# Kernel tuning notes

Hardware: AMD Instinct MI355X
Metric: run time of the kernel (lower is better)

The kernel has to match this reference:

```python
import jax, jax.numpy as jnp
import numpy as np

N_NODES = 50000
SEQ_LEN = 20
INPUT_DIM = 16
HIDDEN = 128
LATENT = 64
N_EDGES = 800000


def setup_inputs() -> dict:
    key = jax.random.key(0)
    ks = iter(jax.random.split(key, 64))
    def p(shape, scale=0.05):
        return jax.random.normal(next(ks), shape, dtype=jnp.float32) * scale
    inp = {}
    inp['track_sequences'] = jax.random.normal(next(ks), (N_NODES, SEQ_LEN, INPUT_DIM), dtype=jnp.float32)
    inp['edge_index'] = jax.random.randint(next(ks), (2, N_EDGES), 0, N_NODES, dtype=jnp.int64)
    # LSTM (2 layers, torch gate order i,f,g,o)
    inp['lstm_Wih0'] = p((4 * HIDDEN, INPUT_DIM)); inp['lstm_Whh0'] = p((4 * HIDDEN, HIDDEN))
    inp['lstm_bih0'] = p((4 * HIDDEN,));            inp['lstm_bhh0'] = p((4 * HIDDEN,))
    inp['lstm_Wih1'] = p((4 * HIDDEN, HIDDEN));     inp['lstm_Whh1'] = p((4 * HIDDEN, HIDDEN))
    inp['lstm_bih1'] = p((4 * HIDDEN,));            inp['lstm_bhh1'] = p((4 * HIDDEN,))
    # encoder MLP: hidden->hidden->latent
    inp['enc_W1'] = p((HIDDEN, HIDDEN)); inp['enc_b1'] = p((HIDDEN,))
    inp['enc_W2'] = p((HIDDEN, LATENT)); inp['enc_b2'] = p((LATENT,))
    # 3 GCN layers
    inp['gcn_W0'] = p((LATENT, HIDDEN)); inp['gcn_b0'] = p((HIDDEN,))
    inp['gcn_W1'] = p((HIDDEN, HIDDEN)); inp['gcn_b1'] = p((HIDDEN,))
    inp['gcn_W2'] = p((HIDDEN, HIDDEN)); inp['gcn_b2'] = p((HIDDEN,))
    # edge predictor MLP: 2H -> H -> H/2 -> 1 (sigmoid)
    inp['e_W1'] = p((2 * HIDDEN, HIDDEN)); inp['e_b1'] = p((HIDDEN,))
    inp['e_W2'] = p((HIDDEN, HIDDEN // 2)); inp['e_b2'] = p((HIDDEN // 2,))
    inp['e_W3'] = p((HIDDEN // 2, 1)); inp['e_b3'] = p((1,))
    # classifier: H -> H/2 -> 4
    inp['c_W1'] = p((HIDDEN, HIDDEN // 2)); inp['c_b1'] = p((HIDDEN // 2,))
    inp['c_W2'] = p((HIDDEN // 2, 4)); inp['c_b2'] = p((4,))
    # uncertainty: H -> H/2 -> 1 (softplus)
    inp['u_W1'] = p((HIDDEN, HIDDEN // 2)); inp['u_b1'] = p((HIDDEN // 2,))
    inp['u_W2'] = p((HIDDEN // 2, 1)); inp['u_b2'] = p((1,))
    return inp


def _lstm_layer(x, Wih, Whh, bih, bhh):
    # x: [N, T, Din]; torch gate order i, f, g, o
    n, t, _ = x.shape
    h_dim = Whh.shape[1]
    xg = jnp.einsum('ntd,gd->ntg', x, Wih) + bih  # [N, T, 4H] precomputed input part
    def step(carry, xt):
        h, c = carry
        g = xt + h @ Whh.T + bhh
        i, f, gg, o = jnp.split(g, 4, axis=-1)
        c = jax.nn.sigmoid(f) * c + jax.nn.sigmoid(i) * jnp.tanh(gg)
        h = jax.nn.sigmoid(o) * jnp.tanh(c)
        return (h, c), h
    h0 = jnp.zeros((n, h_dim), x.dtype)
    (_, _), hs = jax.lax.scan(step, (h0, h0), jnp.swapaxes(xg, 0, 1))
    return jnp.swapaxes(hs, 0, 1)  # [N, T, H]


def _gcn(x, W, b, src, dst, num_nodes):
    # PyG GCNConv: self-loops, symmetric deg^-1/2 normalization
    x = x @ W  # [N, out]
    loop = jnp.arange(num_nodes, dtype=src.dtype)
    s = jnp.concatenate([src, loop])
    d = jnp.concatenate([dst, loop])
    deg = jax.ops.segment_sum(jnp.ones_like(d, x.dtype), d, num_segments=num_nodes)
    dinv = jax.lax.rsqrt(jnp.maximum(deg, 1.0))  # deg >= 1 due to self-loops
    norm = dinv[s] * dinv[d]  # [E+N]
    out = jax.ops.segment_sum(x[s] * norm[:, None], d, num_segments=num_nodes)
    return out + b


def reference(track_sequences, edge_index,
              lstm_Wih0, lstm_Whh0, lstm_bih0, lstm_bhh0,
              lstm_Wih1, lstm_Whh1, lstm_bih1, lstm_bhh1,
              enc_W1, enc_b1, enc_W2, enc_b2,
              gcn_W0, gcn_b0, gcn_W1, gcn_b1, gcn_W2, gcn_b2,
              e_W1, e_b1, e_W2, e_b2, e_W3, e_b3,
              c_W1, c_b1, c_W2, c_b2,
              u_W1, u_b1, u_W2, u_b2):
    n = track_sequences.shape[0]
    # --- TrackEncoder (eval mode: LSTM inter-layer dropout inactive) ---
    h = _lstm_layer(track_sequences, lstm_Wih0, lstm_Whh0, lstm_bih0, lstm_bhh0)
    h = _lstm_layer(h, lstm_Wih1, lstm_Whh1, lstm_bih1, lstm_bhh1)
    final_hidden = h[:, -1]  # [N, H]
    latent = jax.nn.relu(final_hidden @ enc_W1 + enc_b1) @ enc_W2 + enc_b2  # [N, L]
    # --- GCN stack (eval mode: dropout inactive) ---
    src, dst = edge_index[0], edge_index[1]
    x = latent
    for W, b in ((gcn_W0, gcn_b0), (gcn_W1, gcn_b1), (gcn_W2, gcn_b2)):
        x = jax.nn.relu(_gcn(x, W, b, src, dst, n))
    # --- edge predictor ---
    ef = jnp.concatenate([x[src], x[dst]], axis=1)  # [E, 2H]
    ef = jax.nn.relu(ef @ e_W1 + e_b1)
    ef = jax.nn.relu(ef @ e_W2 + e_b2)
    edge_pred = jax.nn.sigmoid(ef @ e_W3 + e_b3)  # [E, 1]
    # --- classifier & uncertainty heads ---
    track_classes = jax.nn.relu(x @ c_W1 + c_b1) @ c_W2 + c_b2  # [N, 4]
    uncertainties = jax.nn.softplus(jax.nn.relu(x @ u_W1 + u_b1) @ u_W2 + u_b2)  # [N, 1]
    return (x, edge_pred, track_classes, uncertainties)
```

## Files before the change

### kernel.cpp

```cpp
#include <hip/hip_runtime.h>
#include <math.h>

typedef float f32x4 __attribute__((ext_vector_type(4)));
typedef short s16x8 __attribute__((ext_vector_type(8)));
typedef unsigned short u16;

__device__ __forceinline__ float sigmoid_(float x) { return 1.f / (1.f + __expf(-x)); }
__device__ __forceinline__ float tanh_(float x) {
  float e = __expf(-2.f * x);
  return fmaf(2.f, 1.f / (1.f + e), -1.f);
}
__device__ __forceinline__ float softplus_(float x) {
  return (x > 15.f) ? x : log1pf(__expf(x));
}
__device__ __forceinline__ u16 f2bf(float f) {
  unsigned u = __float_as_uint(f);
  u += 0x7fffu + ((u >> 16) & 1u);
  return (u16)(u >> 16);
}
__device__ __forceinline__ float bf2f(u16 u) {
  return __uint_as_float((unsigned)u << 16);
}
#define PIN4(x) asm volatile("" : "+v"(x))

__global__ void prep_lstm_w(const float* __restrict__ Wih0, const float* __restrict__ Whh0,
                            const float* __restrict__ Wih1, const float* __restrict__ Whh1,
                            const float* __restrict__ bih0, const float* __restrict__ bhh0,
                            const float* __restrict__ bih1, const float* __restrict__ bhh1,
                            u16* __restrict__ Wp0, u16* __restrict__ Wp1,
                            float* __restrict__ bs0, float* __restrict__ bs1)
{
  int idx = blockIdx.x * 256 + threadIdx.x;
  if (idx < 20 * 512 * 8) {
    int c = idx >> 12, rem = idx & 4095;
    int col = rem >> 3, e = rem & 7;
    int k = c * 8 + e;
    float v = 0.f;
    if (k < 16) v = Wih0[col * 16 + k];
    else if (k >= 32) v = Whh0[col * 128 + (k - 32)];
    Wp0[idx] = f2bf(v);
  }
  int i1 = idx - 20 * 512 * 8;
  if (i1 >= 0 && i1 < 32 * 512 * 8) {
    int c = i1 >> 12, rem = i1 & 4095;
    int col = rem >> 3, e = rem & 7;
    int k = c * 8 + e;
    float v = (k < 128) ? Wih1[col * 128 + k] : Whh1[col * 128 + (k - 128)];
    Wp1[i1] = f2bf(v);
  }
  int i2 = idx - 52 * 512 * 8;
  if (i2 >= 0 && i2 < 512) bs0[i2] = bih0[i2] + bhh0[i2];
  int i3 = i2 - 512;
  if (i3 >= 0 && i3 < 512) bs1[i3] = bih1[i3] + bhh1[i3];
}

__global__ void pack_w(const float* __restrict__ W, u16* __restrict__ Wp, int K, int C) {
  int idx = blockIdx.x * 256 + threadIdx.x;
  if (idx < K * C) {
    int k = idx / C, col = idx % C;
    Wp[((size_t)(k >> 3) * C + col) * 8 + (k & 7)] = f2bf(W[idx]);
  }
}

__global__ void pack_headw(const float* __restrict__ cW1, const float* __restrict__ cb1,
                           const float* __restrict__ cW2, const float* __restrict__ cb2,
                           const float* __restrict__ uW1, const float* __restrict__ ub1,
                           const float* __restrict__ uW2, const float* __restrict__ ub2,
                           u16* __restrict__ cuW1p, float* __restrict__ cub1,
                           u16* __restrict__ cuW2p, float* __restrict__ cub2)
{
  int idx = blockIdx.x * 256 + threadIdx.x;
  if (idx < 128 * 128) {
    int k = idx >> 7, col = idx & 127;
    float v = (col < 64) ? cW1[k * 64 + col] : uW1[k * 64 + (col - 64)];
    cuW1p[((size_t)(k >> 3) * 128 + col) * 8 + (k & 7)] = f2bf(v);
  }
  int j = idx - 128 * 128;
  if (j >= 0 && j < 2048) {
    int ch = j >> 7, rem = j & 127, col = rem >> 3, e = rem & 7;
    int k = ch * 8 + e;
    float v = 0.f;
    if (col < 4 && k < 64) v = cW2[k * 4 + col];
    else if (col == 4 && k >= 64) v = uW2[k - 64];
    cuW2p[j] = f2bf(v);
  }
  int j2 = idx - (128 * 128 + 2048);
  if (j2 >= 0 && j2 < 128) cub1[j2] = (j2 < 64) ? cb1[j2] : ub1[j2 - 64];
  int j3 = j2 - 128;
  if (j3 >= 0 && j3 < 16) cub2[j3] = (j3 < 4) ? cb2[j3] : (j3 == 4 ? ub2[0] : 0.f);
}

__device__ __forceinline__ void epi2(const f32x4 (&acc)[2][4], f32x4* cs,
    const float (&bs)[4], u16* ldsw, int uoff, int kq, int mh,
    int nodebase, float* hf, int u, int n, bool last)
{
#pragma unroll
  for (int mm = 0; mm < 2; ++mm) {
#pragma unroll
    for (int r = 0; r < 4; ++r) {
      float gi = acc[mm][0][r] + bs[0];
      float gf = acc[mm][1][r] + bs[1];
      float gg = acc[mm][2][r] + bs[2];
      float go = acc[mm][3][r] + bs[3];
      float c = sigmoid_(gf) * cs[mm][r] + sigmoid_(gi) * tanh_(gg);
      cs[mm][r] = c;
      float h = sigmoid_(go) * tanh_(c);
      int node = (mh * 2 + mm) * 16 + kq * 4 + r;
      ldsw[uoff + node * 8] = f2bf(h);
      if (last) {
        int gn = nodebase + node;
        if (gn < n) hf[(size_t)gn * 128 + u] = h;
      }
    }
  }
}

__global__ __launch_bounds__(512, 2) void lstm_l0(
    const float* __restrict__ seq, const u16* __restrict__ Wp0,
    const float* __restrict__ bs0, u16* __restrict__ h0seq,
    int n, int tile0, int ntiles)
{
  __shared__ __align__(16) u16 A0[2 * 20 * 512];
  const int RSZ = 20 * 512;
  const int tid = threadIdx.x;
  const int l = tid & 63;
  const int wq = __builtin_amdgcn_readfirstlane(tid >> 6);
  const int kq = l >> 4;
  const int la = (l & 15) * 8;
  const int colu = wq * 16 + (l & 15);
  const int uoff = (4 + (colu >> 3)) * 512 + (colu & 7);

  s16x8 b0[5][4];
#pragma unroll
  for (int kc = 0; kc < 5; ++kc)
#pragma unroll
    for (int g = 0; g < 4; ++g) {
      b0[kc][g] = *(const s16x8*)&Wp0[(size_t)(kc * 4 + kq) * 4096 + (g * 128 + colu) * 8];
      PIN4(b0[kc][g]);
    }
  float bsr[4];
#pragma unroll
  for (int g = 0; g < 4; ++g) bsr[g] = bs0[g * 128 + colu];
  const f32x4 zero4 = {0.f, 0.f, 0.f, 0.f};

  for (int tt = blockIdx.x; tt < ntiles; tt += gridDim.x) {
    const int nodebase = (tile0 + tt) * 64;
    const int nld = min(nodebase + (tid >> 2), n - 1);
    u16* __restrict__ hdst = h0seq + (size_t)tt * 20 * 8192;
    for (int i = tid; i < 18 * 512; i += 512) A0[2 * 512 + i] = 0;
    for (int i = tid; i < 2 * 512; i += 512) A0[RSZ + 2 * 512 + i] = 0;
    if (tid < 256) {
      int nd = tid >> 2, q = tid & 3;
      f32x4 v = __builtin_nontemporal_load((const f32x4*)(seq + (size_t)nld * 320 + q * 4));
      unsigned d0 = (unsigned)f2bf(v[0]) | ((unsigned)f2bf(v[1]) << 16);
      unsigned d1 = (unsigned)f2bf(v[2]) | ((unsigned)f2bf(v[3]) << 16);
      unsigned* dstp = (unsigned*)&A0[(q >> 1) * 512 + nd * 8 + (q & 1) * 4];
      dstp[0] = d0; dstp[1] = d1;
    }
    f32x4 c0[4];
#pragma unroll
    for (int m = 0; m < 4; ++m) c0[m] = zero4;
    __syncthreads();

    for (int t = 0; t < 20; ++t) {
      const int base_r = (t & 1) * RSZ;
      const int base_w = ((t + 1) & 1) * RSZ;
      f32x4 xnext;
      const bool ldx = (t < 19) && (tid < 256);
      if (ldx) xnext = __builtin_nontemporal_load(
          (const f32x4*)(seq + (size_t)nld * 320 + (t + 1) * 16 + (tid & 3) * 4));
      if (t >= 1) {
        s16x8 u0 = *(const s16x8*)&A0[base_r + 2048 + tid * 8];
        s16x8 u1 = *(const s16x8*)&A0[base_r + 2048 + 4096 + tid * 8];
        __builtin_nontemporal_store(u0, (s16x8*)&hdst[(size_t)(t - 1) * 8192 + tid * 8]);
        __builtin_nontemporal_store(u1, (s16x8*)&hdst[(size_t)(t - 1) * 8192 + 4096 + tid * 8]);
      }
#pragma unroll
      for (int mh = 0; mh < 2; ++mh) {
        f32x4 acc[2][4];
#pragma unroll
        for (int mm = 0; mm < 2; ++mm)
#pragma unroll
          for (int g = 0; g < 4; ++g) acc[mm][g] = zero4;
#pragma unroll
        for (int kc = 0; kc < 5; ++kc) {
          const int ch = kc * 4 + kq;
          s16x8 av[2];
#pragma unroll
          for (int mm = 0; mm < 2; ++mm)
            av[mm] = *(const s16x8*)&A0[base_r + ch * 512 + (mh * 2 + mm) * 128 + la];
#pragma unroll
          for (int g = 0; g < 4; ++g)
#pragma unroll
            for (int mm = 0; mm < 2; ++mm)
              acc[mm][g] = __builtin_amdgcn_mfma_f32_16x16x32_bf16(av[mm], b0[kc][g], acc[mm][g], 0, 0, 0);
        }
        epi2(acc, &c0[mh * 2], bsr, &A0[base_w], uoff, kq, mh, 0, nullptr, colu, 0, false);
      }
      if (ldx) {
        int nd = tid >> 2, q = tid & 3;
        unsigned d0 = (unsigned)f2bf(xnext[0]) | ((unsigned)f2bf(xnext[1]) << 16);
        unsigned d1 = (unsigned)f2bf(xnext[2]) | ((unsigned)f2bf(xnext[3]) << 16);
        unsigned* dstp = (unsigned*)&A0[base_w + (q >> 1) * 512 + nd * 8 + (q & 1) * 4];
        dstp[0] = d0; dstp[1] = d1;
      }
      __syncthreads();
    }
    {
      s16x8 u0 = *(const s16x8*)&A0[2048 + tid * 8];
      s16x8 u1 = *(const s16x8*)&A0[2048 + 4096 + tid * 8];
      __builtin_nontemporal_store(u0, (s16x8*)&hdst[(size_t)19 * 8192 + tid * 8]);
      __builtin_nontemporal_store(u1, (s16x8*)&hdst[(size_t)19 * 8192 + 4096 + tid * 8]);
    }
    __syncthreads();
  }
}

__global__ __launch_bounds__(512, 2) void lstm_l1(
    const u16* __restrict__ h0seq, const u16* __restrict__ Wp1,
    const float* __restrict__ bs1, float* __restrict__ hfinal,
    int n, int tile0, int ntiles)
{
  __shared__ __align__(16) u16 A1[2 * 32 * 512];
  const int RSZ = 32 * 512;
  const int tid = threadIdx.x;
  const int l = tid & 63;
  const int wq = __builtin_amdgcn_readfirstlane(tid >> 6);
  const int kq = l >> 4;
  const int la = (l & 15) * 8;
  const int colu = wq * 16 + (l & 15);
  const int uoff = (16 + (colu >> 3)) * 512 + (colu & 7);

  s16x8 b1[8][4];
#pragma unroll
  for (int kc = 0; kc < 8; ++kc)
#pragma unroll
    for (int g = 0; g < 4; ++g) {
      b1[kc][g] = *(const s16x8*)&Wp1[(size_t)(kc * 4 + kq) * 4096 + (g * 128 + colu) * 8];
      PIN4(b1[kc][g]);
    }
  float bsr[4];
#pragma unroll
  for (int g = 0; g < 4; ++g) bsr[g] = bs1[g * 128 + colu];
  const f32x4 zero4 = {0.f, 0.f, 0.f, 0.f};

  for (int tt = blockIdx.x; tt < ntiles; tt += gridDim.x) {
    const int nodebase = (tile0 + tt) * 64;
    const u16* __restrict__ hsrc = h0seq + (size_t)tt * 20 * 8192;
    for (int i = tid; i < 16 * 512; i += 512) A1[16 * 512 + i] = 0;
    {
      s16x8 s0 = __builtin_nontemporal_load((const s16x8*)&hsrc[tid * 8]);
      s16x8 s1 = __builtin_nontemporal_load((const s16x8*)&hsrc[4096 + tid * 8]);
      *(s16x8*)&A1[tid * 8] = s0;
      *(s16x8*)&A1[4096 + tid * 8] = s1;
    }
    f32x4 c1[4];
#pragma unroll
    for (int m = 0; m < 4; ++m) c1[m] = zero4;
    __syncthreads();

    for (int t = 0; t < 20; ++t) {
      const int base_r = (t & 1) * RSZ;
      const int base_w = ((t + 1) & 1) * RSZ;
      s16x8 p0, p1;
      const bool ld = (t < 19);
      if (ld) {
        p0 = __builtin_nontemporal_load((const s16x8*)&hsrc[(size_t)(t + 1) * 8192 + tid * 8]);
        p1 = __builtin_nontemporal_load((const s16x8*)&hsrc[(size_t)(t + 1) * 8192 + 4096 + tid * 8]);
      }
#pragma unroll
      for (int mh = 0; mh < 2; ++mh) {
        f32x4 acc[2][4];
#pragma unroll
        for (int mm = 0; mm < 2; ++mm)
#pragma unroll
          for (int g = 0; g < 4; ++g) acc[mm][g] = zero4;
#pragma unroll
        for (int kc = 0; kc < 8; ++kc) {
          const int ch = kc * 4 + kq;
          s16x8 av[2];
#pragma unroll
          for (int mm = 0; mm < 2; ++mm)
            av[mm] = *(const s16x8*)&A1[base_r + ch * 512 + (mh * 2 + mm) * 128 + la];
#pragma unroll
          for (int g = 0; g < 4; ++g)
#pragma unroll
            for (int mm = 0; mm < 2; ++mm)
              acc[mm][g] = __builtin_amdgcn_mfma_f32_16x16x32_bf16(av[mm], b1[kc][g], acc[mm][g], 0, 0, 0);
        }
        epi2(acc, &c1[mh * 2], bsr, &A1[base_w], uoff, kq, mh, nodebase, hfinal, colu, n, t == 19);
      }
      if (ld) {
        *(s16x8*)&A1[base_w + tid * 8] = p0;
        *(s16x8*)&A1[base_w + 4096 + tid * 8] = p1;
      }
      __syncthreads();
    }
  }
}

template<int KD, int COLS, bool INBF, bool OUTBF, bool RELU, bool BIAS>
__global__ __launch_bounds__(COLS * 4, 4) void ngemm_m(
    const void* __restrict__ xin_, const u16* __restrict__ Wp,
    const float* __restrict__ b, void* __restrict__ out_, int n)
{
  constexpr int NT = COLS * 4;
  __shared__ __align__(16) u16 A[(KD / 8) * 512];
  const int tid = threadIdx.x;
  const int l = tid & 63;
  const int wq = __builtin_amdgcn_readfirstlane(tid >> 6);
  const int kq = l >> 4;
  const int la = (l & 15) * 8;
  const int colu = wq * 16 + (l & 15);
  const int nodebase = blockIdx.x * 64;

  for (int s = tid; s < 64 * KD / 8; s += NT) {
    int nd = s / (KD / 8), q = s % (KD / 8);
    int gn = min(nodebase + nd, n - 1);
    if (INBF) {
      const u16* xp = (const u16*)xin_ + (size_t)gn * KD + q * 8;
      *(s16x8*)&A[q * 512 + nd * 8] = *(const s16x8*)xp;
    } else {
      const float* xp = (const float*)xin_ + (size_t)gn * KD + q * 8;
      float4 v0 = *(const float4*)xp;
      float4 v1 = *(const float4*)(xp + 4);
      s16x8 pk;
      pk[0] = (short)f2bf(v0.x); pk[1] = (short)f2bf(v0.y);
      pk[2] = (short)f2bf(v0.z); pk[3] = (short)f2bf(v0.w);
      pk[4] = (short)f2bf(v1.x); pk[5] = (short)f2bf(v1.y);
      pk[6] = (short)f2bf(v1.z); pk[7] = (short)f2bf(v1.w);
      *(s16x8*)&A[q * 512 + nd * 8] = pk;
    }
  }
  __syncthreads();

  const f32x4 zero4 = {0.f, 0.f, 0.f, 0.f};
  f32x4 acc[4];
#pragma unroll
  for (int m = 0; m < 4; ++m) acc[m] = zero4;
#pragma unroll
  for (int kc = 0; kc < KD / 32; ++kc) {
    const int ch = kc * 4 + kq;
    s16x8 bv = *(const s16x8*)&Wp[((size_t)ch * COLS + colu) * 8];
#pragma unroll
    for (int m = 0; m < 4; ++m) {
      s16x8 av = *(const s16x8*)&A[ch * 512 + m * 128 + la];
      acc[m] = __builtin_amdgcn_mfma_f32_16x16x32_bf16(av, bv, acc[m], 0, 0, 0);
    }
  }
  float bb = BIAS ? b[colu] : 0.f;
#pragma unroll
  for (int m = 0; m < 4; ++m)
#pragma unroll
    for (int r = 0; r < 4; ++r) {
      int gn = nodebase + m * 16 + kq * 4 + r;
      if (gn < n) {
        float v = acc[m][r] + bb;
        if (RELU) v = fmaxf(v, 0.f);
        if (OUTBF) ((u16*)out_)[(size_t)gn * COLS + colu] = f2bf(v);
        else       ((float*)out_)[(size_t)gn * COLS + colu] = v;
      }
    }
}

__global__ void deg_count(const int* __restrict__ dst, float* __restrict__ deg, int ne, int n) {
  int i = blockIdx.x * 256 + threadIdx.x;
  if (i < ne) {
    int d = dst[i]; d = min(max(d, 0), n - 1);
    atomicAdd(deg + d, 1.f);
  }
}

__global__ void dinv_k(const float* __restrict__ deg, float* __restrict__ dinv, int n) {
  int i = blockIdx.x * 256 + threadIdx.x;
  if (i < n) dinv[i] = rsqrtf(deg[i] + 1.f);
}

__global__ void scan_part(const float* __restrict__ deg, int* __restrict__ part, int n) {
  __shared__ int sh[256];
  const int tid = threadIdx.x;
  const int base = blockIdx.x * 1024;
  int s = 0;
  for (int j = tid; j < 1024; j += 256) {
    int i = base + j;
    s += (i < n) ? (int)deg[i] : 0;
  }
  sh[tid] = s;
  __syncthreads();
  for (int off = 128; off > 0; off >>= 1) {
    if (tid < off) sh[tid] += sh[tid + off];
    __syncthreads();
  }
  if (tid == 0) part[blockIdx.x] = sh[0];
}

__global__ void scan_exc(int* __restrict__ part, int nb, int* __restrict__ rowptr, int n) {
  __shared__ int sh[256];
  const int tid = threadIdx.x;
  int v = (tid < nb) ? part[tid] : 0;
  sh[tid] = v;
  __syncthreads();
  for (int off = 1; off < 256; off <<= 1) {
    int t = (tid >= off) ? sh[tid - off] : 0;
    __syncthreads();
    sh[tid] += t;
    __syncthreads();
  }
  if (tid < nb) part[tid] = sh[tid] - v;
  if (tid == 255) rowptr[n] = sh[255];
}

__global__ void scan_final(const float* __restrict__ deg, const int* __restrict__ part,
                           int* __restrict__ rowptr, int n) {
  __shared__ int sh[1024];
  const int tid = threadIdx.x;
  const int i = blockIdx.x * 1024 + tid;
  int v = (i < n) ? (int)deg[i] : 0;
  sh[tid] = v;
  __syncthreads();
  for (int off = 1; off < 1024; off <<= 1) {
    int t = (tid >= off) ? sh[tid - off] : 0;
    __syncthreads();
    sh[tid] += t;
    __syncthreads();
  }
  if (i < n) rowptr[i] = part[blockIdx.x] + sh[tid] - v;
}

__global__ void fill_k(const int* __restrict__ src, const int* __restrict__ dst,
                       const int* __restrict__ rowptr, int* __restrict__ cursor,
                       const float* __restrict__ dinv,
                       int* __restrict__ cidx, float* __restrict__ enrm, int ne, int n) {
  int i = blockIdx.x * 256 + threadIdx.x;
  if (i < ne) {
    int s = min(max(src[i], 0), n - 1);
    int d = min(max(dst[i], 0), n - 1);
    int p = atomicAdd(cursor + d, 1);
    int o = rowptr[d] + p;
    cidx[o] = s;
    enrm[o] = dinv[s] * dinv[d];
  }
}

template<bool OUT32>
__global__ __launch_bounds__(256, 4) void gcn_gather_bf(
    const u16* __restrict__ y, const int* __restrict__ rowptr,
    const int* __restrict__ cidx, const float* __restrict__ enrm,
    const float* __restrict__ dinv, const float* __restrict__ b,
    void* __restrict__ out, int n)
{
  const int l = threadIdx.x & 63;
  const int wq = threadIdx.x >> 6;
  const int node = blockIdx.x * 4 + wq;
  if (node >= n) return;
  float dv = dinv[node];
  unsigned su = ((const unsigned*)(y + (size_t)node * 128))[l];
  float ax = bf2f((u16)(su & 0xffff)) * dv * dv;
  float ay = bf2f((u16)(su >> 16)) * dv * dv;
  int r0 = rowptr[node], r1 = rowptr[node + 1];
  int e = r0;
  for (; e + 1 < r1; e += 2) {
    int s0 = cidx[e], s1 = cidx[e + 1];
    float n0 = enrm[e], n1 = enrm[e + 1];
    unsigned u0 = ((const unsigned*)(y + (size_t)s0 * 128))[l];
    unsigned u1 = ((const unsigned*)(y + (size_t)s1 * 128))[l];
    ax = fmaf(n0, bf2f((u16)(u0 & 0xffff)), ax);
    ay = fmaf(n0, bf2f((u16)(u0 >> 16)), ay);
    ax = fmaf(n1, bf2f((u16)(u1 & 0xffff)), ax);
    ay = fmaf(n1, bf2f((u16)(u1 >> 16)), ay);
  }
  if (e < r1) {
    int s0 = cidx[e];
    float n0 = enrm[e];
    unsigned u0 = ((const unsigned*)(y + (size_t)s0 * 128))[l];
    ax = fmaf(n0, bf2f((u16)(u0 & 0xffff)), ax);
    ay = fmaf(n0, bf2f((u16)(u0 >> 16)), ay);
  }
  float2 bb = *(const float2*)(b + l * 2);
  float ox = fmaxf(ax + bb.x, 0.f);
  float oy = fmaxf(ay + bb.y, 0.f);
  if (OUT32) {
    float2 o; o.x = ox; o.y = oy;
    *(float2*)((float*)out + (size_t)node * 128 + l * 2) = o;
  } else {
    unsigned pk = (unsigned)f2bf(ox) | ((unsigned)f2bf(oy) << 16);
    ((unsigned*)((u16*)out + (size_t)node * 128))[l] = pk;
  }
}

__global__ __launch_bounds__(256, 4) void gather64_k(
    const float* __restrict__ y, const int* __restrict__ rowptr,
    const int* __restrict__ cidx, const float* __restrict__ enrm,
    const float* __restrict__ dinv, float* __restrict__ out, int n)
{
  const int l = threadIdx.x & 63;
  const int wq = threadIdx.x >> 6;
  const int node = blockIdx.x * 4 + wq;
  if (node >= n) return;
  float dv = dinv[node];
  float acc = y[(size_t)node * 64 + l] * dv * dv;
  int r0 = rowptr[node], r1 = rowptr[node + 1];
  int e = r0;
  for (; e + 1 < r1; e += 2) {
    int s0 = cidx[e], s1 = cidx[e + 1];
    float n0 = enrm[e], n1 = enrm[e + 1];
    acc = fmaf(n0, y[(size_t)s0 * 64 + l], acc);
    acc = fmaf(n1, y[(size_t)s1 * 64 + l], acc);
  }
  if (e < r1) acc = fmaf(enrm[e], y[(size_t)cidx[e] * 64 + l], acc);
  out[(size_t)node * 64 + l] = acc;
}

__global__ __launch_bounds__(256, 4) void edge_head_m(
    const u16* __restrict__ P, const u16* __restrict__ Q,
    const int* __restrict__ src, const int* __restrict__ dst,
    const float* __restrict__ b1, const u16* __restrict__ eW2p,
    const float* __restrict__ b2, const float* __restrict__ eW3,
    const float* __restrict__ b3, float* __restrict__ ep, int ne, int n)
{
  __shared__ __align__(16) u16 H1f[16 * 512];
  __shared__ float Hpart[64][4];
  const int tid = threadIdx.x;
  const int l = tid & 63;
  const int w = __builtin_amdgcn_readfirstlane(tid >> 6);
  const int kq = l >> 4;
  const int la = (l & 15) * 8;
  const int col = w * 16 + (l & 15);
  const int e0 = blockIdx.x * 64;
  {
    int el = tid >> 2, q = tid & 3;
    int e = min(e0 + el, ne - 1);
    int s = min(max(src[e], 0), n - 1);
    int d = min(max(dst[e], 0), n - 1);
    const u16* pr = P + (size_t)s * 128 + q * 32;
    const u16* qr = Q + (size_t)d * 128 + q * 32;
#pragma unroll
    for (int c = 0; c < 4; ++c) {
      s16x8 pv = *(const s16x8*)(pr + c * 8);
      s16x8 qv = *(const s16x8*)(qr + c * 8);
      s16x8 hv;
#pragma unroll
      for (int i = 0; i < 8; ++i) {
        float h = bf2f((u16)pv[i]) + bf2f((u16)qv[i]) + b1[q * 32 + c * 8 + i];
        hv[i] = (short)f2bf(fmaxf(h, 0.f));
      }
      *(s16x8*)&H1f[(q * 4 + c) * 512 + el * 8] = hv;
    }
  }
  __syncthreads();
  const f32x4 zero4 = {0.f, 0.f, 0.f, 0.f};
  f32x4 acc[4];
#pragma unroll
  for (int m = 0; m < 4; ++m) acc[m] = zero4;
#pragma unroll
  for (int kc = 0; kc < 4; ++kc) {
    int ch = kc * 4 + kq;
    s16x8 bv = *(const s16x8*)&eW2p[((size_t)ch * 64 + col) * 8];
#pragma unroll
    for (int m = 0; m < 4; ++m) {
      s16x8 av = *(const s16x8*)&H1f[ch * 512 + m * 128 + la];
      acc[m] = __builtin_amdgcn_mfma_f32_16x16x32_bf16(av, bv, acc[m], 0, 0, 0);
    }
  }
  const float w3 = eW3[col];
  const float b2c = b2[col];
#pragma unroll
  for (int m = 0; m < 4; ++m)
#pragma unroll
    for (int r = 0; r < 4; ++r) {
      float v = fmaxf(acc[m][r] + b2c, 0.f) * w3;
      v += __shfl_xor(v, 1);
      v += __shfl_xor(v, 2);
      v += __shfl_xor(v, 4);
      v += __shfl_xor(v, 8);
      if ((l & 15) == 0) Hpart[m * 16 + kq * 4 + r][w] = v;
    }
  __syncthreads();
  if (tid < 64) {
    float s = Hpart[tid][0] + Hpart[tid][1] + Hpart[tid][2] + Hpart[tid][3] + b3[0];
    int e = e0 + tid;
    if (e < ne) ep[e] = 1.f / (1.f + __expf(-s));
  }
}

__global__ __launch_bounds__(512, 2) void node_heads_m(
    const float* __restrict__ x, const u16* __restrict__ cuW1p,
    const float* __restrict__ cub1, const u16* __restrict__ cuW2p,
    const float* __restrict__ cub2, float* __restrict__ cls,
    float* __restrict__ unc, int n)
{
  __shared__ __align__(16) u16 A[16 * 512];
  __shared__ __align__(16) u16 Hf[16 * 512];
  const int tid = threadIdx.x;
  const int l = tid & 63;
  const int wq = __builtin_amdgcn_readfirstlane(tid >> 6);
  const int kq = l >> 4;
  const int la = (l & 15) * 8;
  const int col = wq * 16 + (l & 15);
  const int nodebase = blockIdx.x * 64;

  for (int s = tid; s < 1024; s += 512) {
    int nd = s >> 4, q = s & 15;
    int gn = min(nodebase + nd, n - 1);
    const float* xp = x + (size_t)gn * 128 + q * 8;
    float4 v0 = *(const float4*)xp;
    float4 v1 = *(const float4*)(xp + 4);
    s16x8 pk;
    pk[0] = (short)f2bf(v0.x); pk[1] = (short)f2bf(v0.y);
    pk[2] = (short)f2bf(v0.z); pk[3] = (short)f2bf(v0.w);
    pk[4] = (short)f2bf(v1.x); pk[5] = (short)f2bf(v1.y);
    pk[6] = (short)f2bf(v1.z); pk[7] = (short)f2bf(v1.w);
    *(s16x8*)&A[q * 512 + nd * 8] = pk;
  }
  __syncthreads();

  const f32x4 zero4 = {0.f, 0.f, 0.f, 0.f};
  f32x4 acc[4];
#pragma unroll
  for (int m = 0; m < 4; ++m) acc[m] = zero4;
#pragma unroll
  for (int kc = 0; kc < 4; ++kc) {
    int ch = kc * 4 + kq;
    s16x8 bv = *(const s16x8*)&cuW1p[((size_t)ch * 128 + col) * 8];
#pragma unroll
    for (int m = 0; m < 4; ++m) {
      s16x8 av = *(const s16x8*)&A[ch * 512 + m * 128 + la];
      acc[m] = __builtin_amdgcn_mfma_f32_16x16x32_bf16(av, bv, acc[m], 0, 0, 0);
    }
  }
  const float bb = cub1[col];
#pragma unroll
  for (int m = 0; m < 4; ++m)
#pragma unroll
    for (int r = 0; r < 4; ++r) {
      float h = fmaxf(acc[m][r] + bb, 0.f);
      int node_r = m * 16 + kq * 4 + r;
      Hf[(col >> 3) * 512 + node_r * 8 + (col & 7)] = f2bf(h);
    }
  __syncthreads();
  if (wq == 0) {
    f32x4 a2[4];
#pragma unroll
    for (int m = 0; m < 4; ++m) a2[m] = zero4;
    const int col2 = l & 15;
#pragma unroll
    for (int kc = 0; kc < 4; ++kc) {
      int ch = kc * 4 + kq;
      s16x8 bv = *(const s16x8*)&cuW2p[((size_t)ch * 16 + col2) * 8];
#pragma unroll
      for (int m = 0; m < 4; ++m) {
        s16x8 av = *(const s16x8*)&Hf[ch * 512 + m * 128 + la];
        a2[m] = __builtin_amdgcn_mfma_f32_16x16x32_bf16(av, bv, a2[m], 0, 0, 0);
      }
    }
    const float b2v = cub2[col2];
#pragma unroll
    for (int m = 0; m < 4; ++m)
#pragma unroll
      for (int r = 0; r < 4; ++r) {
        int node = nodebase + m * 16 + kq * 4 + r;
        if (node < n) {
          float v = a2[m][r] + b2v;
          if (col2 < 4) cls[(size_t)node * 4 + col2] = v;
          else if (col2 == 4) unc[node] = softplus_(v);
        }
      }
  }
}

extern "C" void kernel_launch(void* const* d_in, const int* in_sizes, int n_in,
                              void* d_out, int out_size, void* d_ws, size_t ws_size,
                              hipStream_t stream)
{
  const float* seq   = (const float*)d_in[0];
  const int*   eidx  = (const int*)d_in[1];
  const float* Wih0  = (const float*)d_in[2];
  const float* Whh0  = (const float*)d_in[3];
  const float* bih0  = (const float*)d_in[4];
  const float* bhh0  = (const float*)d_in[5];
  const float* Wih1  = (const float*)d_in[6];
  const float* Whh1  = (const float*)d_in[7];
  const float* bih1  = (const float*)d_in[8];
  const float* bhh1  = (const float*)d_in[9];
  const float* encW1 = (const float*)d_in[10];
  const float* encb1 = (const float*)d_in[11];
  const float* encW2 = (const float*)d_in[12];
  const float* encb2 = (const float*)d_in[13];
  const float* gW0   = (const float*)d_in[14];
  const float* gb0   = (const float*)d_in[15];
  const float* gW1   = (const float*)d_in[16];
  const float* gb1   = (const float*)d_in[17];
  const float* gW2   = (const float*)d_in[18];
  const float* gb2   = (const float*)d_in[19];
  const float* eW1   = (const float*)d_in[20];
  const float* eb1   = (const float*)d_in[21];
  const float* eW2   = (const float*)d_in[22];
  const float* eb2   = (const float*)d_in[23];
  const float* eW3   = (const float*)d_in[24];
  const float* eb3   = (const float*)d_in[25];
  const float* cW1   = (const float*)d_in[26];
  const float* cb1   = (const float*)d_in[27];
  const float* cW2   = (const float*)d_in[28];
  const float* cb2   = (const float*)d_in[29];
  const float* uW1   = (const float*)d_in[30];
  const float* ub1   = (const float*)d_in[31];
  const float* uW2   = (const float*)d_in[32];
  const float* ub2   = (const float*)d_in[33];

  const int n  = in_sizes[0] / 320;
  const int ne = in_sizes[1] / 2;
  const int* src = eidx;
  const int* dst = eidx + ne;

  char* ws = (char*)d_ws;
  size_t off = 0;
  auto alloc = [&](size_t elems) -> float* {
    float* p = (float*)(ws + off);
    off += ((elems * 4 + 255) & ~(size_t)255);
    return p;
  };
  const size_t nb = (size_t)n * 128;
  float* B1     = alloc(nb);
  float* B2     = alloc(nb);
  float* B4     = alloc(nb);
  float* latent = alloc((size_t)n * 64);
  float* deg    = alloc(n);
  float* dinv   = alloc(n);
  int*   rowptr = (int*)alloc(n + 1);
  int*   cursor = (int*)alloc(n);
  int*   part   = (int*)alloc(256);
  int*   cidx   = (int*)alloc(ne);
  float* enrm   = alloc(ne);
  u16* Wp0    = (u16*)alloc(20 * 512 * 8 / 2);
  u16* Wp1    = (u16*)alloc(32 * 512 * 8 / 2);
  u16* encW1p = (u16*)alloc(128 * 128 / 2);
  u16* encW2p = (u16*)alloc(128 * 64 / 2);
  u16* gW0p   = (u16*)alloc(64 * 128 / 2);
  u16* gW1p   = (u16*)alloc(128 * 128 / 2);
  u16* gW2p   = (u16*)alloc(128 * 128 / 2);
  u16* eW1tp  = (u16*)alloc(128 * 128 / 2);
  u16* eW1bp  = (u16*)alloc(128 * 128 / 2);
  u16* eW2p   = (u16*)alloc(128 * 64 / 2);
  u16* cuW1p  = (u16*)alloc(128 * 128 / 2);
  u16* cuW2p  = (u16*)alloc(1024);
  float* cub1  = alloc(128);
  float* cub2  = alloc(16);
  float* bsum0 = alloc(512);
  float* bsum1 = alloc(512);
  (void)n_in; (void)out_size;

  float* xout = (float*)d_out;
  float* ep   = xout + nb;
  float* cls  = ep + ne;
  float* unc  = cls + (size_t)n * 4;

  auto PK = [&](const float* s, u16* d, int K, int C) {
    pack_w<<<dim3((K * C + 255) / 256), dim3(256), 0, stream>>>(s, d, K, C);
  };
  PK(encW1, encW1p, 128, 128);
  PK(encW2, encW2p, 128, 64);
  PK(gW0,   gW0p,   64, 128);
  PK(gW1,   gW1p,   128, 128);
  PK(gW2,   gW2p,   128, 128);
  PK(eW1,             eW1tp, 128, 128);
  PK(eW1 + 128 * 128, eW1bp, 128, 128);
  PK(eW2,   eW2p,   128, 64);
  pack_headw<<<dim3((128 * 128 + 2048 + 128 + 16 + 255) / 256), dim3(256), 0, stream>>>(
      cW1, cb1, cW2, cb2, uW1, ub1, uW2, ub2, cuW1p, cub1, cuW2p, cub2);

  prep_lstm_w<<<dim3((52 * 512 * 8 + 1024 + 255) / 256), dim3(256), 0, stream>>>(
      Wih0, Whh0, Wih1, Whh1, bih0, bhh0, bih1, bhh1, Wp0, Wp1, bsum0, bsum1);

  hipMemsetAsync(deg, 0, (size_t)n * 4, stream);
  deg_count<<<dim3((ne + 255) / 256), dim3(256), 0, stream>>>(dst, deg, ne, n);
  dinv_k<<<dim3((n + 255) / 256), dim3(256), 0, stream>>>(deg, dinv, n);
  const int nsb = (n + 1023) / 1024;
  scan_part<<<dim3(nsb), dim3(256), 0, stream>>>(deg, part, n);
  scan_exc<<<dim3(1), dim3(256), 0, stream>>>(part, nsb, rowptr, n);
  scan_final<<<dim3(nsb), dim3(1024), 0, stream>>>(deg, part, rowptr, n);
  hipMemsetAsync(cursor, 0, (size_t)n * 4, stream);
  fill_k<<<dim3((ne + 255) / 256), dim3(256), 0, stream>>>(
      src, dst, rowptr, cursor, dinv, cidx, enrm, ne, n);

  const int nblk = (n + 63) / 64;
  const int ntiles = nblk;

  const size_t per_tile = (size_t)20 * 8192 * sizeof(u16);
  size_t avail = (ws_size > off) ? (ws_size - off) : 0;
  int slab_tiles = (int)((avail / per_tile < (size_t)ntiles) ? (avail / per_tile) : (size_t)ntiles);
  if (slab_tiles < 1) slab_tiles = 1;
  {
    u16* h0seq = (u16*)(ws + off);
    for (int t0 = 0; t0 < ntiles; t0 += slab_tiles) {
      int st = (ntiles - t0 < slab_tiles) ? (ntiles - t0) : slab_tiles;
      int grid = (st < 512) ? st : 512;
      lstm_l0<<<dim3(grid), dim3(512), 0, stream>>>(seq, Wp0, bsum0, h0seq, n, t0, st);
      lstm_l1<<<dim3(grid), dim3(512), 0, stream>>>(h0seq, Wp1, bsum1, B1, n, t0, st);
    }
  }

  u16* t1b = (u16*)B2;
  u16* xb  = (u16*)B1;
  u16* yb  = (u16*)B2;
  u16* xb2 = (u16*)B4;
  u16* Pb  = (u16*)B1;
  u16* Qb  = (u16*)B4;
  ngemm_m<128, 128, false, true, true, true><<<dim3(nblk), dim3(512), 0, stream>>>(B1, encW1p, encb1, t1b, n);
  ngemm_m<128, 64, true, false, false, true><<<dim3(nblk), dim3(256), 0, stream>>>(t1b, encW2p, encb2, latent, n);

  const int gblk = (n + 3) / 4;
  gather64_k<<<dim3(gblk), dim3(256), 0, stream>>>(latent, rowptr, cidx, enrm, dinv, B2, n);
  ngemm_m<64, 128, false, true, true, true><<<dim3(nblk), dim3(512), 0, stream>>>(B2, gW0p, gb0, xb, n);
  ngemm_m<128, 128, true, true, false, false><<<dim3(nblk), dim3(512), 0, stream>>>(xb, gW1p, nullptr, yb, n);
  gcn_gather_bf<false><<<dim3(gblk), dim3(256), 0, stream>>>(yb, rowptr, cidx, enrm, dinv, gb1, xb2, n);
  ngemm_m<128, 128, true, true, false, false><<<dim3(nblk), dim3(512), 0, stream>>>(xb2, gW2p, nullptr, yb, n);
  gcn_gather_bf<true><<<dim3(gblk), dim3(256), 0, stream>>>(yb, rowptr, cidx, enrm, dinv, gb2, xout, n);

  ngemm_m<128, 128, false, true, false, false><<<dim3(nblk), dim3(512), 0, stream>>>(xout, eW1tp, nullptr, Pb, n);
  ngemm_m<128, 128, false, true, false, false><<<dim3(nblk), dim3(512), 0, stream>>>(xout, eW1bp, nullptr, Qb, n);
  edge_head_m<<<dim3((ne + 63) / 64), dim3(256), 0, stream>>>(
      Pb, Qb, src, dst, eb1, eW2p, eb2, eW3, eb3, ep, ne, n);

  node_heads_m<<<dim3(nblk), dim3(512), 0, stream>>>(
      xout, cuW1p, cub1, cuW2p, cub2, cls, unc, n);
}
```

Baseline: 1.946 ms.

## Process edge head in CSR dst-sorted order and store latent as bf16

```diff
diff --git a/kernel.cpp b/kernel.cpp
--- a/kernel.cpp
+++ b/kernel.cpp
@@ -430,7 +430,8 @@
 __global__ void fill_k(const int* __restrict__ src, const int* __restrict__ dst,
                        const int* __restrict__ rowptr, int* __restrict__ cursor,
                        const float* __restrict__ dinv,
-                       int* __restrict__ cidx, float* __restrict__ enrm, int ne, int n) {
+                       int* __restrict__ cidx, int* __restrict__ dnode,
+                       int* __restrict__ eorig, float* __restrict__ enrm, int ne, int n) {
   int i = blockIdx.x * 256 + threadIdx.x;
   if (i < ne) {
     int s = min(max(src[i], 0), n - 1);
@@ -438,6 +439,8 @@
     int p = atomicAdd(cursor + d, 1);
     int o = rowptr[d] + p;
     cidx[o] = s;
+    dnode[o] = d;
+    eorig[o] = i;
     enrm[o] = dinv[s] * dinv[d];
   }
 }
@@ -488,8 +491,8 @@
   }
 }
 
-__global__ __launch_bounds__(256, 4) void gather64_k(
-    const float* __restrict__ y, const int* __restrict__ rowptr,
+__global__ __launch_bounds__(256, 4) void gather64_bf(
+    const u16* __restrict__ y, const int* __restrict__ rowptr,
     const int* __restrict__ cidx, const float* __restrict__ enrm,
     const float* __restrict__ dinv, float* __restrict__ out, int n)
 {
@@ -498,22 +501,23 @@
   const int node = blockIdx.x * 4 + wq;
   if (node >= n) return;
   float dv = dinv[node];
-  float acc = y[(size_t)node * 64 + l] * dv * dv;
+  float acc = bf2f(y[(size_t)node * 64 + l]) * dv * dv;
   int r0 = rowptr[node], r1 = rowptr[node + 1];
   int e = r0;
   for (; e + 1 < r1; e += 2) {
     int s0 = cidx[e], s1 = cidx[e + 1];
     float n0 = enrm[e], n1 = enrm[e + 1];
-    acc = fmaf(n0, y[(size_t)s0 * 64 + l], acc);
-    acc = fmaf(n1, y[(size_t)s1 * 64 + l], acc);
-  }
-  if (e < r1) acc = fmaf(enrm[e], y[(size_t)cidx[e] * 64 + l], acc);
+    acc = fmaf(n0, bf2f(y[(size_t)s0 * 64 + l]), acc);
+    acc = fmaf(n1, bf2f(y[(size_t)s1 * 64 + l]), acc);
+  }
+  if (e < r1) acc = fmaf(enrm[e], bf2f(y[(size_t)cidx[e] * 64 + l]), acc);
   out[(size_t)node * 64 + l] = acc;
 }
 
 __global__ __launch_bounds__(256, 4) void edge_head_m(
     const u16* __restrict__ P, const u16* __restrict__ Q,
-    const int* __restrict__ src, const int* __restrict__ dst,
+    const int* __restrict__ cidx, const int* __restrict__ dnode,
+    const int* __restrict__ eorig,
     const float* __restrict__ b1, const u16* __restrict__ eW2p,
     const float* __restrict__ b2, const float* __restrict__ eW3,
     const float* __restrict__ b3, float* __restrict__ ep, int ne, int n)
@@ -529,9 +533,9 @@
   const int e0 = blockIdx.x * 64;
   {
     int el = tid >> 2, q = tid & 3;
-    int e = min(e0 + el, ne - 1);
-    int s = min(max(src[e], 0), n - 1);
-    int d = min(max(dst[e], 0), n - 1);
+    int o = min(e0 + el, ne - 1);
+    int s = cidx[o];
+    int d = dnode[o];
     const u16* pr = P + (size_t)s * 128 + q * 32;
     const u16* qr = Q + (size_t)d * 128 + q * 32;
 #pragma unroll
@@ -577,9 +581,11 @@
     }
   __syncthreads();
   if (tid < 64) {
-    float s = Hpart[tid][0] + Hpart[tid][1] + Hpart[tid][2] + Hpart[tid][3] + b3[0];
-    int e = e0 + tid;
-    if (e < ne) ep[e] = 1.f / (1.f + __expf(-s));
+    int o = e0 + tid;
+    if (o < ne) {
+      float s = Hpart[tid][0] + Hpart[tid][1] + Hpart[tid][2] + Hpart[tid][3] + b3[0];
+      ep[eorig[o]] = 1.f / (1.f + __expf(-s));
+    }
   }
 }
 
@@ -723,13 +729,15 @@
   float* B1     = alloc(nb);
   float* B2     = alloc(nb);
   float* B4     = alloc(nb);
-  float* latent = alloc((size_t)n * 64);
+  float* latent = alloc((size_t)n * 32);
   float* deg    = alloc(n);
   float* dinv   = alloc(n);
   int*   rowptr = (int*)alloc(n + 1);
   int*   cursor = (int*)alloc(n);
   int*   part   = (int*)alloc(256);
   int*   cidx   = (int*)alloc(ne);
+  int*   dnode  = (int*)alloc(ne);
+  int*   eorig  = (int*)alloc(ne);
   float* enrm   = alloc(ne);
   u16* Wp0    = (u16*)alloc(20 * 512 * 8 / 2);
   u16* Wp1    = (u16*)alloc(32 * 512 * 8 / 2);
@@ -780,7 +788,7 @@
   scan_final<<<dim3(nsb), dim3(1024), 0, stream>>>(deg, part, rowptr, n);
   hipMemsetAsync(cursor, 0, (size_t)n * 4, stream);
   fill_k<<<dim3((ne + 255) / 256), dim3(256), 0, stream>>>(
-      src, dst, rowptr, cursor, dinv, cidx, enrm, ne, n);
+      src, dst, rowptr, cursor, dinv, cidx, dnode, eorig, enrm, ne, n);
 
   const int nblk = (n + 63) / 64;
   const int ntiles = nblk;
@@ -799,17 +807,18 @@
     }
   }
 
-  u16* t1b = (u16*)B2;
-  u16* xb  = (u16*)B1;
-  u16* yb  = (u16*)B2;
-  u16* xb2 = (u16*)B4;
-  u16* Pb  = (u16*)B1;
-  u16* Qb  = (u16*)B4;
+  u16* t1b  = (u16*)B2;
+  u16* latb = (u16*)latent;
+  u16* xb   = (u16*)B1;
+  u16* yb   = (u16*)B2;
+  u16* xb2  = (u16*)B4;
+  u16* Pb   = (u16*)B1;
+  u16* Qb   = (u16*)B4;
   ngemm_m<128, 128, false, true, true, true><<<dim3(nblk), dim3(512), 0, stream>>>(B1, encW1p, encb1, t1b, n);
-  ngemm_m<128, 64, true, false, false, true><<<dim3(nblk), dim3(256), 0, stream>>>(t1b, encW2p, encb2, latent, n);
+  ngemm_m<128, 64, true, true, false, true><<<dim3(nblk), dim3(256), 0, stream>>>(t1b, encW2p, encb2, latb, n);
 
   const int gblk = (n + 3) / 4;
-  gather64_k<<<dim3(gblk), dim3(256), 0, stream>>>(latent, rowptr, cidx, enrm, dinv, B2, n);
+  gather64_bf<<<dim3(gblk), dim3(256), 0, stream>>>(latb, rowptr, cidx, enrm, dinv, B2, n);
   ngemm_m<64, 128, false, true, true, true><<<dim3(nblk), dim3(512), 0, stream>>>(B2, gW0p, gb0, xb, n);
   ngemm_m<128, 128, true, true, false, false><<<dim3(nblk), dim3(512), 0, stream>>>(xb, gW1p, nullptr, yb, n);
   gcn_gather_bf<false><<<dim3(gblk), dim3(256), 0, stream>>>(yb, rowptr, cidx, enrm, dinv, gb1, xb2, n);
@@ -819,7 +828,7 @@
   ngemm_m<128, 128, false, true, false, false><<<dim3(nblk), dim3(512), 0, stream>>>(xout, eW1tp, nullptr, Pb, n);
   ngemm_m<128, 128, false, true, false, false><<<dim3(nblk), dim3(512), 0, stream>>>(xout, eW1bp, nullptr, Qb, n);
   edge_head_m<<<dim3((ne + 63) / 64), dim3(256), 0, stream>>>(
-      Pb, Qb, src, dst, eb1, eW2p, eb2, eW3, eb3, ep, ne, n);
+      Pb, Qb, cidx, dnode, eorig, eb1, eW2p, eb2, eW3, eb3, ep, ne, n);
 
   node_heads_m<<<dim3(nblk), dim3(512), 0, stream>>>(
       xout, cuW1p, cub1, cuW2p, cub2, cls, unc, n);
```

Measured after the change: 1.940 ms. No clear change (-0.3%).
